# Optimization experiments

Measured on AMD Instinct MI355X. Metric: run time of the kernel, lower is better.

## Reference

```python
import jax, jax.numpy as jnp
import numpy as np

N_NODES = 50000
N_EDGES = 800000
IN_FEATS = 128
HEADS = 8
OUT_FEATS = 32
NEG_SLOPE = 0.2


def setup_inputs() -> dict:
    key = jax.random.key(0)
    k_feat, k_w, k_al, k_ar, k_src, k_dst = jax.random.split(key, 6)
    feat = jax.random.normal(k_feat, (N_NODES, IN_FEATS), dtype=jnp.float32)
    W_fc = jax.random.normal(k_w, (HEADS * OUT_FEATS, IN_FEATS), dtype=jnp.float32) * 0.1
    attn_l = jax.random.normal(k_al, (1, HEADS, OUT_FEATS), dtype=jnp.float32) * 0.1
    attn_r = jax.random.normal(k_ar, (1, HEADS, OUT_FEATS), dtype=jnp.float32) * 0.1
    src = jax.random.randint(k_src, (N_EDGES,), 0, N_NODES, dtype=jnp.int32)
    dst = jax.random.randint(k_dst, (N_EDGES,), 0, N_NODES, dtype=jnp.int32)
    return {"feat": feat, "W_fc": W_fc, "attn_l": attn_l, "attn_r": attn_r,
            "src": src, "dst": dst}


def reference(feat, W_fc, attn_l, attn_r, src, dst):
    N = feat.shape[0]
    H, D = attn_l.shape[1], attn_l.shape[2]
    # fc projection: [N, H, D]
    feat_hd = (feat @ W_fc.T).reshape(N, H, D)
    # per-node left/right attention logits: [N, H]
    el = (feat_hd * attn_l).sum(-1)
    er = (feat_hd * attn_r).sum(-1)
    # u_add_v gather -> per-edge score [E, H], then leaky relu
    e = el[src] + er[dst]
    e = jnp.where(e > 0, e, NEG_SLOPE * e)
    # edge softmax: segment softmax over edges grouped by dst node
    m = jax.ops.segment_max(e, dst, num_segments=N)        # [N, H]
    a = jnp.exp(e - m[dst])                                # [E, H]
    z = jax.ops.segment_sum(a, dst, num_segments=N)        # [N, H]
    a = a / z[dst]
    # u_mul_e + sum: weighted scatter-aggregation -> [N, H, D]
    msg = feat_hd[src] * a[:, :, None]                     # [E, H, D]
    out = jax.ops.segment_sum(msg, dst, num_segments=N)
    return out
```

## Files before the change

kernel.cpp:

```cpp
#include <hip/hip_runtime.h>

#define N_NODES_C 50000
#define N_EDGES_C 800000
#define IN_FEATS_C 128
#define HEADS_C 8
#define HD_C 256
#define NEG_SLOPE_C 0.2f
#define SCAN_NBLK 49
#define LDT 136

#define GEMM_BLOCKS 782
#define DEG_BLOCKS 242
#define K1_GRID (GEMM_BLOCKS + DEG_BLOCKS)

typedef __attribute__((ext_vector_type(8))) short bf16x8;
typedef __attribute__((ext_vector_type(4))) float floatx4;

__device__ inline unsigned short f2bf(float f) {
  unsigned int u = __float_as_uint(f);
  unsigned int r = (u + 0x7FFFu + ((u >> 16) & 1u)) >> 16;
  return (unsigned short)r;
}
__device__ inline float bf2f(unsigned short s) {
  unsigned int u = ((unsigned int)s) << 16;
  return __uint_as_float(u);
}

__device__ inline void boff_scan(const int* __restrict__ bsum, int* sboff) {
  int t = threadIdx.x;
  if (t < 64) {
    int own = (t < SCAN_NBLK) ? bsum[t] : 0;
    int v = own;
#pragma unroll
    for (int off = 1; off < 64; off <<= 1) {
      int u = __shfl_up(v, off);
      if (t >= off) v += u;
    }
    sboff[t] = v - own;
  }
  __syncthreads();
}

__global__ __launch_bounds__(256) void front_kernel(
    const float* __restrict__ feat, const float* __restrict__ W,
    const float* __restrict__ attn_l, const float* __restrict__ attn_r,
    const int* __restrict__ dst,
    unsigned short* __restrict__ feat_hd_bf,
    float* __restrict__ el, float* __restrict__ er,
    int* __restrict__ deg, int* __restrict__ rank) {
  __shared__ __align__(16) unsigned short sA[128 * LDT];
  __shared__ float sAttnL[128];
  __shared__ float sAttnR[128];
  const int bid = blockIdx.x;
  const int t = threadIdx.x;

  if (bid < DEG_BLOCKS) {
    for (int e0 = (bid * 256 + t) * 8; e0 < N_EDGES_C; e0 += DEG_BLOCKS * 2048) {
      int4 da = *(const int4*)&dst[e0];
      int4 db = *(const int4*)&dst[e0 + 4];
      int r0 = atomicAdd(&deg[da.x], 1);
      int r1 = atomicAdd(&deg[da.y], 1);
      int r2 = atomicAdd(&deg[da.z], 1);
      int r3 = atomicAdd(&deg[da.w], 1);
      int r4 = atomicAdd(&deg[db.x], 1);
      int r5 = atomicAdd(&deg[db.y], 1);
      int r6 = atomicAdd(&deg[db.z], 1);
      int r7 = atomicAdd(&deg[db.w], 1);
      *(int4*)&rank[e0]     = make_int4(r0, r1, r2, r3);
      *(int4*)&rank[e0 + 4] = make_int4(r4, r5, r6, r7);
    }
    return;
  }

  const int gb = bid - DEG_BLOCKS;
  const int nt = gb & 1;
  const int mt = gb >> 1;
  const int m0 = mt * 128;
  const int n0 = nt * 128;

  if (t < 128) {
    sAttnL[t] = attn_l[n0 + t];
    sAttnR[t] = attn_r[n0 + t];
  }
#pragma unroll
  for (int i = 0; i < 16; ++i) {
    int idx = t + i * 256;
    int row = idx >> 5;
    int c4 = idx & 31;
    int gn = m0 + row;
    float4 v = (gn < N_NODES_C)
                   ? *(const float4*)&feat[(size_t)gn * IN_FEATS_C + c4 * 4]
                   : make_float4(0.f, 0.f, 0.f, 0.f);
    ushort4 b;
    b.x = f2bf(v.x); b.y = f2bf(v.y); b.z = f2bf(v.z); b.w = f2bf(v.w);
    *(ushort4*)&sA[row * LDT + c4 * 4] = b;
  }
  __syncthreads();

  const int wid = t >> 6;
  const int lane = t & 63;
  const int quad = lane >> 4;
  const int l16 = lane & 15;
  const int wm = (wid & 1) * 64;
  const int wn = (wid >> 1) * 64;

  floatx4 acc[4][4];
#pragma unroll
  for (int i = 0; i < 4; ++i)
#pragma unroll
    for (int j = 0; j < 4; ++j) acc[i][j] = (floatx4){0.f, 0.f, 0.f, 0.f};

#pragma unroll
  for (int ks = 0; ks < 4; ++ks) {
    int k0 = ks * 32 + quad * 8;
    bf16x8 bfv[4];
#pragma unroll
    for (int n2 = 0; n2 < 4; ++n2) {
      const float* wp = &W[(size_t)(n0 + wn + n2 * 16 + l16) * IN_FEATS_C + k0];
      float4 w0 = *(const float4*)wp;
      float4 w1 = *(const float4*)(wp + 4);
      bf16x8 b;
      b[0] = (short)f2bf(w0.x); b[1] = (short)f2bf(w0.y);
      b[2] = (short)f2bf(w0.z); b[3] = (short)f2bf(w0.w);
      b[4] = (short)f2bf(w1.x); b[5] = (short)f2bf(w1.y);
      b[6] = (short)f2bf(w1.z); b[7] = (short)f2bf(w1.w);
      bfv[n2] = b;
    }
    bf16x8 af[4];
#pragma unroll
    for (int m2 = 0; m2 < 4; ++m2)
      af[m2] = *(const bf16x8*)&sA[(wm + m2 * 16 + l16) * LDT + k0];
#pragma unroll
    for (int m2 = 0; m2 < 4; ++m2)
#pragma unroll
      for (int n2 = 0; n2 < 4; ++n2)
        acc[m2][n2] = __builtin_amdgcn_mfma_f32_16x16x32_bf16(
            af[m2], bfv[n2], acc[m2][n2], 0, 0, 0);
  }
  __syncthreads();

#pragma unroll
  for (int m2 = 0; m2 < 4; ++m2)
#pragma unroll
    for (int n2 = 0; n2 < 4; ++n2)
#pragma unroll
      for (int r = 0; r < 4; ++r) {
        int row = wm + m2 * 16 + quad * 4 + r;
        int col = wn + n2 * 16 + l16;
        sA[row * LDT + col] = f2bf(acc[m2][n2][r]);
      }
  __syncthreads();

#pragma unroll
  for (int i = 0; i < 8; ++i) {
    int idx = t + i * 256;
    int row = idx >> 4;
    int ch = idx & 15;
    int gn = m0 + row;
    if (gn < N_NODES_C) {
      *(uint4*)&feat_hd_bf[(size_t)gn * HD_C + n0 + ch * 8] =
          *(const uint4*)&sA[row * LDT + ch * 8];
    }
  }

  {
    int row = t >> 1;
    int hh = t & 1;
    int gn = m0 + row;
    if (gn < N_NODES_C) {
      const unsigned short* pr = &sA[row * LDT + hh * 64];
      const float* al = &sAttnL[hh * 64];
      const float* ar = &sAttnR[hh * 64];
      float el0 = 0.f, el1 = 0.f, er0 = 0.f, er1 = 0.f;
#pragma unroll
      for (int d = 0; d < 32; ++d) {
        float v0 = bf2f(pr[d]);
        float v1 = bf2f(pr[32 + d]);
        el0 = fmaf(v0, al[d], el0);
        er0 = fmaf(v0, ar[d], er0);
        el1 = fmaf(v1, al[32 + d], el1);
        er1 = fmaf(v1, ar[32 + d], er1);
      }
      int gh = nt * 4 + hh * 2;
      el[gn * HEADS_C + gh + 0] = el0;
      el[gn * HEADS_C + gh + 1] = el1;
      er[gn * HEADS_C + gh + 0] = er0;
      er[gn * HEADS_C + gh + 1] = er1;
    }
  }
}

__global__ __launch_bounds__(256) void scan1_kernel(
    const int* __restrict__ deg, int* __restrict__ row_start,
    int* __restrict__ bsum) {
  __shared__ int s[256];
  int b = blockIdx.x, t = threadIdx.x;
  int i0 = b * 1024 + t * 4;
  int d0 = 0, d1 = 0, d2 = 0, d3 = 0;
  if (i0 + 4 <= N_NODES_C) {
    int4 d = *(const int4*)&deg[i0];
    d0 = d.x; d1 = d.y; d2 = d.z; d3 = d.w;
  } else {
    if (i0 + 0 < N_NODES_C) d0 = deg[i0 + 0];
    if (i0 + 1 < N_NODES_C) d1 = deg[i0 + 1];
    if (i0 + 2 < N_NODES_C) d2 = deg[i0 + 2];
    if (i0 + 3 < N_NODES_C) d3 = deg[i0 + 3];
  }
  int l1 = d0, l2 = l1 + d1, l3 = l2 + d2, l4 = l3 + d3;
  s[t] = l4;
  __syncthreads();
#pragma unroll
  for (int off = 1; off < 256; off <<= 1) {
    int add = (t >= off) ? s[t - off] : 0;
    __syncthreads();
    s[t] += add;
    __syncthreads();
  }
  int excl = s[t] - l4;
  if (i0 + 0 < N_NODES_C) row_start[i0 + 0] = excl + l1;
  if (i0 + 1 < N_NODES_C) row_start[i0 + 1] = excl + l2;
  if (i0 + 2 < N_NODES_C) row_start[i0 + 2] = excl + l3;
  if (i0 + 3 < N_NODES_C) row_start[i0 + 3] = excl + l4;
  if (t == 255) bsum[b] = s[255];
}

__global__ __launch_bounds__(256) void scatter_kernel(
    const int* __restrict__ src, const int* __restrict__ dst,
    const int* __restrict__ row_start, const int* __restrict__ deg,
    const int* __restrict__ bsum, const int* __restrict__ rank,
    int* __restrict__ csr_src) {
  __shared__ int sboff[64];
  boff_scan(bsum, sboff);
  int e = blockIdx.x * 256 + threadIdx.x;
  if (e >= N_EDGES_C) return;
  int d = dst[e];
  int pos = row_start[d] - deg[d] + sboff[d >> 10] + rank[e];
  csr_src[pos] = src[e];
}

__global__ __launch_bounds__(256) void agg_csr_kernel(
    const unsigned short* __restrict__ feat_hd_bf, const float* __restrict__ el,
    const float* __restrict__ er, const int* __restrict__ row_start,
    const int* __restrict__ deg, const int* __restrict__ bsum,
    const int* __restrict__ csr_src, float* __restrict__ out) {
  __shared__ int sboff[64];
  boff_scan(bsum, sboff);
  int gid = blockIdx.x * 256 + threadIdx.x;
  int node = gid >> 6;
  int lane = threadIdx.x & 63;
  if (node >= N_NODES_C) return;
  int h = lane >> 3;
  int j8 = lane & 7;
  int hbase = lane & 56;
  int c = lane * 4;
  float er_d = er[node * HEADS_C + h];
  int dg = deg[node];
  int rs = row_start[node] - dg + sboff[node >> 10];
  float4 acc = make_float4(0.f, 0.f, 0.f, 0.f);
  float zsum = 0.f;

  int nb = (dg + 7) >> 3;
  if (nb > 0) {
    int myidx = csr_src[rs + min(j8, dg - 1)];
    for (int b = 0; b < nb; ++b) {
      int e0 = b * 8;
      ushort4 f[8];
#pragma unroll
      for (int j = 0; j < 8; ++j) {
        int sj = __shfl(myidx, j);
        f[j] = *(const ushort4*)&feat_hd_bf[(size_t)sj * HD_C + c];
      }
      float x = el[myidx * HEADS_C + h] + er_d;
      x = x > 0.f ? x : NEG_SLOPE_C * x;
      float wv = (e0 + j8 < dg) ? __expf(x) : 0.f;
      int nidx = csr_src[rs + min(e0 + 8 + j8, dg - 1)];
      float wj[8];
#pragma unroll
      for (int j = 0; j < 8; ++j) wj[j] = __shfl(wv, hbase + j);
      zsum += ((wj[0] + wj[1]) + (wj[2] + wj[3])) +
              ((wj[4] + wj[5]) + (wj[6] + wj[7]));
#pragma unroll
      for (int j = 0; j < 8; ++j) {
        acc.x = fmaf(wj[j], bf2f(f[j].x), acc.x);
        acc.y = fmaf(wj[j], bf2f(f[j].y), acc.y);
        acc.z = fmaf(wj[j], bf2f(f[j].z), acc.z);
        acc.w = fmaf(wj[j], bf2f(f[j].w), acc.w);
      }
      myidx = nidx;
    }
  }

  float inv = (dg > 0) ? 1.f / zsum : 0.f;
  acc.x *= inv; acc.y *= inv; acc.z *= inv; acc.w *= inv;
  *(float4*)&out[(size_t)node * HD_C + c] = acc;
}

extern "C" void kernel_launch(void* const* d_in, const int* in_sizes, int n_in,
                              void* d_out, int out_size, void* d_ws, size_t ws_size,
                              hipStream_t stream) {
  const float* feat   = (const float*)d_in[0];
  const float* W      = (const float*)d_in[1];
  const float* attn_l = (const float*)d_in[2];
  const float* attn_r = (const float*)d_in[3];
  const int* src      = (const int*)d_in[4];
  const int* dst      = (const int*)d_in[5];
  float* out = (float*)d_out;

  char* ws = (char*)d_ws;
  unsigned short* feat_hd_bf = (unsigned short*)ws;  ws += (size_t)N_NODES_C * HD_C * 2;
  float* el      = (float*)ws;                       ws += (size_t)N_NODES_C * HEADS_C * 4;
  float* er      = (float*)ws;                       ws += (size_t)N_NODES_C * HEADS_C * 4;
  int* deg       = (int*)ws;                         ws += (size_t)N_NODES_C * 4;
  int* row_start = (int*)ws;                         ws += (size_t)N_NODES_C * 4;
  int* bsum      = (int*)ws;                         ws += 64 * 4;
  int* csr_src   = (int*)ws;                         ws += (size_t)N_EDGES_C * 4;
  int* rank      = (int*)ws;                         ws += (size_t)N_EDGES_C * 4;

  hipMemsetAsync(deg, 0, (size_t)N_NODES_C * 4, stream);

  front_kernel<<<K1_GRID, 256, 0, stream>>>(feat, W, attn_l, attn_r, dst,
                                            feat_hd_bf, el, er, deg, rank);

  scan1_kernel<<<SCAN_NBLK, 256, 0, stream>>>(deg, row_start, bsum);

  scatter_kernel<<<(N_EDGES_C + 255) / 256, 256, 0, stream>>>(
      src, dst, row_start, deg, bsum, rank, csr_src);

  agg_csr_kernel<<<(N_NODES_C + 3) / 4, 256, 0, stream>>>(
      feat_hd_bf, el, er, row_start, deg, bsum, csr_src, out);
}
```

Measured before the change: 231.2 us.

## Double-buffer neighbor gathers in aggregation and pack row start with degree

The aggregation loop is rewritten to process two 8-edge blocks per iteration. It prefetches the next block's feature rows, el values and CSR indices while computing the current block, to hide gather latency. Row start and degree are packed into one int2 array so the scatter and aggregation kernels need one load instead of two. Nontemporal hints are added to the feat load, the feat_hd store and the output store. The nontemporal store of feat_hd may cost cache reuse, since aggregation reads it again right away.

Result: slower. 247.5 us (+7.0%).

```diff
diff --git a/kernel.cpp b/kernel.cpp
--- a/kernel.cpp
+++ b/kernel.cpp
@@ -15,6 +15,7 @@
 
 typedef __attribute__((ext_vector_type(8))) short bf16x8;
 typedef __attribute__((ext_vector_type(4))) float floatx4;
+typedef __attribute__((ext_vector_type(4))) unsigned int uintx4;
 
 __device__ inline unsigned short f2bf(float f) {
   unsigned int u = __float_as_uint(f);
@@ -88,11 +89,12 @@
     int row = idx >> 5;
     int c4 = idx & 31;
     int gn = m0 + row;
-    float4 v = (gn < N_NODES_C)
-                   ? *(const float4*)&feat[(size_t)gn * IN_FEATS_C + c4 * 4]
-                   : make_float4(0.f, 0.f, 0.f, 0.f);
+    floatx4 v = (floatx4){0.f, 0.f, 0.f, 0.f};
+    if (gn < N_NODES_C)
+      v = __builtin_nontemporal_load(
+          (const floatx4*)&feat[(size_t)gn * IN_FEATS_C + c4 * 4]);
     ushort4 b;
-    b.x = f2bf(v.x); b.y = f2bf(v.y); b.z = f2bf(v.z); b.w = f2bf(v.w);
+    b.x = f2bf(v[0]); b.y = f2bf(v[1]); b.z = f2bf(v[2]); b.w = f2bf(v[3]);
     *(ushort4*)&sA[row * LDT + c4 * 4] = b;
   }
   __syncthreads();
@@ -158,8 +160,9 @@
     int ch = idx & 15;
     int gn = m0 + row;
     if (gn < N_NODES_C) {
-      *(uint4*)&feat_hd_bf[(size_t)gn * HD_C + n0 + ch * 8] =
-          *(const uint4*)&sA[row * LDT + ch * 8];
+      uintx4 v = *(const uintx4*)&sA[row * LDT + ch * 8];
+      __builtin_nontemporal_store(
+          v, (uintx4*)&feat_hd_bf[(size_t)gn * HD_C + n0 + ch * 8]);
     }
   }
 
@@ -191,7 +194,7 @@
 }
 
 __global__ __launch_bounds__(256) void scan1_kernel(
-    const int* __restrict__ deg, int* __restrict__ row_start,
+    const int* __restrict__ deg, int2* __restrict__ rsd,
     int* __restrict__ bsum) {
   __shared__ int s[256];
   int b = blockIdx.x, t = threadIdx.x;
@@ -217,32 +220,32 @@
     __syncthreads();
   }
   int excl = s[t] - l4;
-  if (i0 + 0 < N_NODES_C) row_start[i0 + 0] = excl + l1;
-  if (i0 + 1 < N_NODES_C) row_start[i0 + 1] = excl + l2;
-  if (i0 + 2 < N_NODES_C) row_start[i0 + 2] = excl + l3;
-  if (i0 + 3 < N_NODES_C) row_start[i0 + 3] = excl + l4;
+  if (i0 + 0 < N_NODES_C) rsd[i0 + 0] = make_int2(excl + l1, d0);
+  if (i0 + 1 < N_NODES_C) rsd[i0 + 1] = make_int2(excl + l2, d1);
+  if (i0 + 2 < N_NODES_C) rsd[i0 + 2] = make_int2(excl + l3, d2);
+  if (i0 + 3 < N_NODES_C) rsd[i0 + 3] = make_int2(excl + l4, d3);
   if (t == 255) bsum[b] = s[255];
 }
 
 __global__ __launch_bounds__(256) void scatter_kernel(
     const int* __restrict__ src, const int* __restrict__ dst,
-    const int* __restrict__ row_start, const int* __restrict__ deg,
-    const int* __restrict__ bsum, const int* __restrict__ rank,
-    int* __restrict__ csr_src) {
+    const int2* __restrict__ rsd, const int* __restrict__ bsum,
+    const int* __restrict__ rank, int* __restrict__ csr_src) {
   __shared__ int sboff[64];
   boff_scan(bsum, sboff);
   int e = blockIdx.x * 256 + threadIdx.x;
   if (e >= N_EDGES_C) return;
   int d = dst[e];
-  int pos = row_start[d] - deg[d] + sboff[d >> 10] + rank[e];
+  int2 v = rsd[d];
+  int pos = v.x - v.y + sboff[d >> 10] + rank[e];
   csr_src[pos] = src[e];
 }
 
 __global__ __launch_bounds__(256) void agg_csr_kernel(
     const unsigned short* __restrict__ feat_hd_bf, const float* __restrict__ el,
-    const float* __restrict__ er, const int* __restrict__ row_start,
-    const int* __restrict__ deg, const int* __restrict__ bsum,
-    const int* __restrict__ csr_src, float* __restrict__ out) {
+    const float* __restrict__ er, const int2* __restrict__ rsd,
+    const int* __restrict__ bsum, const int* __restrict__ csr_src,
+    float* __restrict__ out) {
   __shared__ int sboff[64];
   boff_scan(bsum, sboff);
   int gid = blockIdx.x * 256 + threadIdx.x;
@@ -254,45 +257,82 @@
   int hbase = lane & 56;
   int c = lane * 4;
   float er_d = er[node * HEADS_C + h];
-  int dg = deg[node];
-  int rs = row_start[node] - dg + sboff[node >> 10];
+  int2 v = rsd[node];
+  int dg = v.y;
+  int rs = v.x - dg + sboff[node >> 10];
   float4 acc = make_float4(0.f, 0.f, 0.f, 0.f);
   float zsum = 0.f;
 
   int nb = (dg + 7) >> 3;
   if (nb > 0) {
-    int myidx = csr_src[rs + min(j8, dg - 1)];
-    for (int b = 0; b < nb; ++b) {
-      int e0 = b * 8;
-      ushort4 f[8];
+    const int last = dg - 1;
+    int idxA = csr_src[rs + min(j8, last)];
+    float elA = el[idxA * HEADS_C + h];
+    ushort4 fA[8];
+#pragma unroll
+    for (int j = 0; j < 8; ++j) {
+      int sj = __shfl(idxA, j);
+      fA[j] = *(const ushort4*)&feat_hd_bf[(size_t)sj * HD_C + c];
+    }
+    int idxB = csr_src[rs + min(8 + j8, last)];
+
+    for (int b = 0; b < nb; b += 2) {
+      float elB = el[idxB * HEADS_C + h];
+      ushort4 fB[8];
 #pragma unroll
       for (int j = 0; j < 8; ++j) {
-        int sj = __shfl(myidx, j);
-        f[j] = *(const ushort4*)&feat_hd_bf[(size_t)sj * HD_C + c];
-      }
-      float x = el[myidx * HEADS_C + h] + er_d;
-      x = x > 0.f ? x : NEG_SLOPE_C * x;
-      float wv = (e0 + j8 < dg) ? __expf(x) : 0.f;
-      int nidx = csr_src[rs + min(e0 + 8 + j8, dg - 1)];
-      float wj[8];
-#pragma unroll
-      for (int j = 0; j < 8; ++j) wj[j] = __shfl(wv, hbase + j);
-      zsum += ((wj[0] + wj[1]) + (wj[2] + wj[3])) +
-              ((wj[4] + wj[5]) + (wj[6] + wj[7]));
+        int sj = __shfl(idxB, j);
+        fB[j] = *(const ushort4*)&feat_hd_bf[(size_t)sj * HD_C + c];
+      }
+      int idxC = csr_src[rs + min((b + 2) * 8 + j8, last)];
+      {
+        float x = elA + er_d;
+        x = x > 0.f ? x : NEG_SLOPE_C * x;
+        float wv = (b * 8 + j8 < dg) ? __expf(x) : 0.f;
+        float wj[8];
+#pragma unroll
+        for (int j = 0; j < 8; ++j) wj[j] = __shfl(wv, hbase + j);
+        zsum += ((wj[0] + wj[1]) + (wj[2] + wj[3])) +
+                ((wj[4] + wj[5]) + (wj[6] + wj[7]));
+#pragma unroll
+        for (int j = 0; j < 8; ++j) {
+          acc.x = fmaf(wj[j], bf2f(fA[j].x), acc.x);
+          acc.y = fmaf(wj[j], bf2f(fA[j].y), acc.y);
+          acc.z = fmaf(wj[j], bf2f(fA[j].z), acc.z);
+          acc.w = fmaf(wj[j], bf2f(fA[j].w), acc.w);
+        }
+      }
+      float elA2 = el[idxC * HEADS_C + h];
 #pragma unroll
       for (int j = 0; j < 8; ++j) {
-        acc.x = fmaf(wj[j], bf2f(f[j].x), acc.x);
-        acc.y = fmaf(wj[j], bf2f(f[j].y), acc.y);
-        acc.z = fmaf(wj[j], bf2f(f[j].z), acc.z);
-        acc.w = fmaf(wj[j], bf2f(f[j].w), acc.w);
-      }
-      myidx = nidx;
+        int sj = __shfl(idxC, j);
+        fA[j] = *(const ushort4*)&feat_hd_bf[(size_t)sj * HD_C + c];
+      }
+      int idxD = csr_src[rs + min((b + 3) * 8 + j8, last)];
+      {
+        float x = elB + er_d;
+        x = x > 0.f ? x : NEG_SLOPE_C * x;
+        float wv = ((b + 1) * 8 + j8 < dg) ? __expf(x) : 0.f;
+        float wj[8];
+#pragma unroll
+        for (int j = 0; j < 8; ++j) wj[j] = __shfl(wv, hbase + j);
+        zsum += ((wj[0] + wj[1]) + (wj[2] + wj[3])) +
+                ((wj[4] + wj[5]) + (wj[6] + wj[7]));
+#pragma unroll
+        for (int j = 0; j < 8; ++j) {
+          acc.x = fmaf(wj[j], bf2f(fB[j].x), acc.x);
+          acc.y = fmaf(wj[j], bf2f(fB[j].y), acc.y);
+          acc.z = fmaf(wj[j], bf2f(fB[j].z), acc.z);
+          acc.w = fmaf(wj[j], bf2f(fB[j].w), acc.w);
+        }
+      }
+      idxA = idxC; elA = elA2; idxB = idxD;
     }
   }
 
   float inv = (dg > 0) ? 1.f / zsum : 0.f;
-  acc.x *= inv; acc.y *= inv; acc.z *= inv; acc.w *= inv;
-  *(float4*)&out[(size_t)node * HD_C + c] = acc;
+  floatx4 ov = (floatx4){acc.x * inv, acc.y * inv, acc.z * inv, acc.w * inv};
+  __builtin_nontemporal_store(ov, (floatx4*)&out[(size_t)node * HD_C + c]);
 }
 
 extern "C" void kernel_launch(void* const* d_in, const int* in_sizes, int n_in,
@@ -311,7 +351,7 @@
   float* el      = (float*)ws;                       ws += (size_t)N_NODES_C * HEADS_C * 4;
   float* er      = (float*)ws;                       ws += (size_t)N_NODES_C * HEADS_C * 4;
   int* deg       = (int*)ws;                         ws += (size_t)N_NODES_C * 4;
-  int* row_start = (int*)ws;                         ws += (size_t)N_NODES_C * 4;
+  int2* rsd      = (int2*)ws;                        ws += (size_t)N_NODES_C * 8;
   int* bsum      = (int*)ws;                         ws += 64 * 4;
   int* csr_src   = (int*)ws;                         ws += (size_t)N_EDGES_C * 4;
   int* rank      = (int*)ws;                         ws += (size_t)N_EDGES_C * 4;
@@ -321,11 +361,11 @@
   front_kernel<<<K1_GRID, 256, 0, stream>>>(feat, W, attn_l, attn_r, dst,
                                             feat_hd_bf, el, er, deg, rank);
 
-  scan1_kernel<<<SCAN_NBLK, 256, 0, stream>>>(deg, row_start, bsum);
+  scan1_kernel<<<SCAN_NBLK, 256, 0, stream>>>(deg, rsd, bsum);
 
   scatter_kernel<<<(N_EDGES_C + 255) / 256, 256, 0, stream>>>(
-      src, dst, row_start, deg, bsum, rank, csr_src);
+      src, dst, rsd, bsum, rank, csr_src);
 
   agg_csr_kernel<<<(N_NODES_C + 3) / 4, 256, 0, stream>>>(
-      feat_hd_bf, el, er, row_start, deg, bsum, csr_src, out);
-}
+      feat_hd_bf, el, er, rsd, bsum, csr_src, out);
+}
```
